# Kernel optimization log

Hardware: AMD Instinct MI355X
Metric: run time of the kernel (lower is better)

## Reference

```python
import jax, jax.numpy as jnp
import numpy as np

N_NODES = 102400
N_EDGES = 1638400
IN_SIZE = 128
OUT_SIZE = 128
G_SIZE = 100


def setup_inputs() -> dict:
    key = jax.random.key(0)
    ks = jax.random.split(key, 8)
    x = jax.random.normal(ks[0], (N_NODES, IN_SIZE), dtype=jnp.float32)
    W1 = jax.random.normal(ks[1], (IN_SIZE, OUT_SIZE), dtype=jnp.float32) * (IN_SIZE ** -0.5)
    b1 = jnp.zeros((OUT_SIZE,), dtype=jnp.float32)
    W2 = jax.random.normal(ks[2], (OUT_SIZE, OUT_SIZE), dtype=jnp.float32) * (OUT_SIZE ** -0.5)
    b2 = jnp.zeros((OUT_SIZE,), dtype=jnp.float32)
    W3 = jax.random.normal(ks[3], (OUT_SIZE, OUT_SIZE), dtype=jnp.float32) * (OUT_SIZE ** -0.5)
    b3 = jnp.zeros((OUT_SIZE,), dtype=jnp.float32)
    edge_src = jax.random.randint(ks[4], (N_EDGES,), 0, N_NODES, dtype=jnp.int64)
    edge_dst = jax.random.randint(ks[5], (N_EDGES,), 0, N_NODES, dtype=jnp.int64)
    return {"x": x, "W1": W1, "b1": b1, "W2": W2, "b2": b2, "W3": W3, "b3": b3,
            "edge_src": edge_src, "edge_dst": edge_dst, "g_size": G_SIZE}


def _degree_norm(idx, n_nodes):
    # DGL norm='both': deg.clamp(min=1) ** -0.5
    deg = jax.ops.segment_sum(jnp.ones(idx.shape, dtype=jnp.float32), idx, num_segments=n_nodes)
    return jnp.maximum(deg, 1.0) ** -0.5  # [N]


def _graph_conv(feat, W, b, edge_src, edge_dst, src_norm, dst_norm):
    # out = D_dst^{-1/2} A (D_src^{-1/2} feat) W + b
    h = feat * src_norm[:, None]                                   # [N, d]
    agg = jax.ops.segment_sum(h[edge_src], edge_dst, num_segments=feat.shape[0])  # SpMM gather+scatter
    agg = agg * dst_norm[:, None]
    return agg @ W + b


def reference(x, W1, b1, W2, b2, W3, b3, edge_src, edge_dst, g_size):
    n = x.shape[0]
    src_norm = _degree_norm(edge_src, n)  # out-degree based
    dst_norm = _degree_norm(edge_dst, n)  # in-degree based

    y1 = jax.nn.elu(_graph_conv(x, W1, b1, edge_src, edge_dst, src_norm, dst_norm))
    y2 = jax.nn.elu(_graph_conv(y1, W2, b2, edge_src, edge_dst, src_norm, dst_norm))
    y3 = jax.nn.softmax(_graph_conv(y2, W3, b3, edge_src, edge_dst, src_norm, dst_norm), axis=1)

    d = y1.shape[-1]
    return (y1.reshape(-1, g_size, d), y2.reshape(-1, g_size, d), y3.reshape(-1, g_size, d))
```

## Files before the change

kernel.cpp:

```cpp
#include <hip/hip_runtime.h>
#include <hip/hip_fp16.h>
#include <cstdint>
#include <cstddef>

#define N_NODES 102400
#define N_EDGES 1638400
#define DIM 128
#define SLOTS 48
#define NB 200
#define BKT_CAP 9216
#define SC_BLOCKS 400
#define SC_EPT 16

typedef _Float16 f16x8 __attribute__((ext_vector_type(8)));
typedef float f32x4 __attribute__((ext_vector_type(4)));


__global__ void k_initcur(int* __restrict__ dstCur, int* __restrict__ srcCur,
                          unsigned short* __restrict__ fbA,
                          unsigned short* __restrict__ fbB) {
  const int i = threadIdx.x;
  if (i < NB) {
    dstCur[i] = i * BKT_CAP;
    srcCur[i] = i * BKT_CAP;
  }
  if (i < 64) {
    reinterpret_cast<unsigned*>(fbA + (size_t)N_NODES * DIM)[i] = 0u;
  } else if (i < 128) {
    reinterpret_cast<unsigned*>(fbB + (size_t)N_NODES * DIM)[i - 64] = 0u;
  }
}

__global__ __launch_bounds__(256) void k_scatter(
    const int* __restrict__ esrc, const int* __restrict__ edst,
    int* __restrict__ dstCur, int* __restrict__ srcCur,
    unsigned* __restrict__ dstStage, unsigned short* __restrict__ srcStage) {
  __shared__ int histD[NB], histS[NB], baseD[NB], baseS[NB], locD[NB], locS[NB];
  const int tid = threadIdx.x;
  const int ebase = blockIdx.x * (256 * SC_EPT);

  for (int i = tid; i < NB; i += 256) {
    histD[i] = 0; histS[i] = 0; locD[i] = 0; locS[i] = 0;
  }
  __syncthreads();

  int s[SC_EPT], d[SC_EPT];
  #pragma unroll
  for (int k = 0; k < SC_EPT; ++k) {
    const int e = ebase + k * 256 + tid;
    s[k] = esrc[e];
    d[k] = edst[e];
    atomicAdd(&histD[d[k] >> 9], 1);
    atomicAdd(&histS[s[k] >> 9], 1);
  }
  __syncthreads();

  for (int i = tid; i < NB; i += 256) {
    baseD[i] = atomicAdd(&dstCur[i], histD[i]);
    baseS[i] = atomicAdd(&srcCur[i], histS[i]);
  }
  __syncthreads();

  #pragma unroll
  for (int k = 0; k < SC_EPT; ++k) {
    const int bd = d[k] >> 9;
    const int od = atomicAdd(&locD[bd], 1);
    dstStage[baseD[bd] + od] = ((unsigned)s[k] << 9) | (unsigned)(d[k] & 511);
    const int bs = s[k] >> 9;
    const int os = atomicAdd(&locS[bs], 1);
    srcStage[baseS[bs] + os] = (unsigned short)(s[k] & 511);
  }
}

__global__ __launch_bounds__(256) void k_csr(
    const unsigned* __restrict__ dstStage, const int* __restrict__ dstCur,
    int* __restrict__ cnt, unsigned* __restrict__ csr) {
  __shared__ int c[512], cur[512];
  const int b = blockIdx.x;
  const int tid = threadIdx.x;
  const int node0 = b * 512;

  const unsigned dummy = (unsigned)N_NODES << 8;
  uint4 dv;
  dv.x = dummy; dv.y = dummy; dv.z = dummy; dv.w = dummy;
  uint4* c4 = reinterpret_cast<uint4*>(csr + (size_t)node0 * SLOTS);
  for (int i = tid; i < 512 * SLOTS / 4; i += 256) c4[i] = dv;

  #pragma unroll
  for (int k = 0; k < 2; ++k) { c[tid + k * 256] = 0; cur[tid + k * 256] = 0; }
  __syncthreads();

  const int base = b * BKT_CAP;
  const int n = dstCur[b] - base;
  for (int i = tid; i < n; i += 256) {
    atomicAdd(&c[dstStage[base + i] & 511], 1);
  }
  __syncthreads();

  #pragma unroll
  for (int k = 0; k < 2; ++k) cnt[node0 + tid + k * 256] = c[tid + k * 256];

  for (int i = tid; i < n; i += 256) {
    const unsigned e = dstStage[base + i];
    const int dloc = (int)(e & 511u);
    const int slot = atomicAdd(&cur[dloc], 1);
    csr[(size_t)(node0 + dloc) * SLOTS + slot] = (e >> 9) << 8;
  }
}

__global__ __launch_bounds__(256) void k_sdeg(
    const unsigned short* __restrict__ srcStage, const int* __restrict__ srcCur,
    int* __restrict__ deg_src) {
  __shared__ int c[512];
  const int b = blockIdx.x;
  const int tid = threadIdx.x;
  #pragma unroll
  for (int k = 0; k < 2; ++k) c[tid + k * 256] = 0;
  __syncthreads();
  const int base = b * BKT_CAP;
  const int n = srcCur[b] - base;
  for (int i = tid; i < n; i += 256) {
    atomicAdd(&c[srcStage[base + i]], 1);
  }
  __syncthreads();
  const int node0 = b * 512;
  #pragma unroll
  for (int k = 0; k < 2; ++k) deg_src[node0 + tid + k * 256] = c[tid + k * 256];
}

__global__ void k_cvt_scale(const float* __restrict__ x,
                            const int* __restrict__ deg_src,
                            unsigned short* __restrict__ out) {
  const int i = blockIdx.x * blockDim.x + threadIdx.x;
  const int row = i >> 5;
  const int dg = deg_src[row];
  const float sn = rsqrtf((float)(dg > 0 ? dg : 1));
  const float4 v = reinterpret_cast<const float4*>(x)[i];
  ushort4 o;
  o.x = __half_as_ushort(__float2half_rn(v.x * sn));
  o.y = __half_as_ushort(__float2half_rn(v.y * sn));
  o.z = __half_as_ushort(__float2half_rn(v.z * sn));
  o.w = __half_as_ushort(__float2half_rn(v.w * sn));
  reinterpret_cast<ushort4*>(out)[i] = o;
}

template <int ACT>
__global__ __launch_bounds__(256, 6) void k_layer_m(
    const unsigned short* __restrict__ fb_in, const float* __restrict__ W,
    const float* __restrict__ bias, const int* __restrict__ cnt,
    const unsigned* __restrict__ csr, const int* __restrict__ deg_src,
    float* __restrict__ out, unsigned short* __restrict__ fb_out) {
  __shared__ float buf[32][132];
  __half* aggH = reinterpret_cast<__half*>(&buf[0][0]);

  const int tid  = threadIdx.x;
  const int lane = tid & 63;
  const int wid  = tid >> 6;
  const int q    = lane >> 4;
  const int li   = lane & 15;
  const int brow = blockIdx.x * 32;
  const char* fbase = reinterpret_cast<const char*>(fb_in);

  int c_[8];
  unsigned pk_[8];
  #pragma unroll
  for (int k = 0; k < 8; ++k) {
    const int gr = brow + wid + 4 * k;
    c_[k] = cnt[gr];
    pk_[k] = (lane < SLOTS) ? csr[(size_t)gr * SLOTS + lane] : 0u;
  }

  #pragma unroll
  for (int pass = 0; pass < 2; ++pass) {
    const int kb = pass * 4;
    __half2 acc[4][4];
    #pragma unroll
    for (int k = 0; k < 4; ++k)
      #pragma unroll
      for (int i = 0; i < 4; ++i) acc[k][i] = __float2half2_rn(0.0f);

    int cmax = c_[kb] > c_[kb + 1] ? c_[kb] : c_[kb + 1];
    cmax = cmax > c_[kb + 2] ? cmax : c_[kb + 2];
    cmax = cmax > c_[kb + 3] ? cmax : c_[kb + 3];
    cmax = cmax > SLOTS ? SLOTS : cmax;
    const int nq = (cmax + 3) >> 2;

    #pragma unroll 2
    for (int j = 0; j < nq; ++j) {
      const int sl = 4 * j + q;
      #pragma unroll
      for (int k = 0; k < 4; ++k) {
        const int o = __shfl((int)pk_[kb + k], sl);
        const uint4 v = *reinterpret_cast<const uint4*>(
            fbase + (size_t)(unsigned)o + (li << 4));
        acc[k][0] = __hadd2(acc[k][0], *reinterpret_cast<const __half2*>(&v.x));
        acc[k][1] = __hadd2(acc[k][1], *reinterpret_cast<const __half2*>(&v.y));
        acc[k][2] = __hadd2(acc[k][2], *reinterpret_cast<const __half2*>(&v.z));
        acc[k][3] = __hadd2(acc[k][3], *reinterpret_cast<const __half2*>(&v.w));
      }
    }

    #pragma unroll
    for (int k = 0; k < 4; ++k) {
      #pragma unroll
      for (int i = 0; i < 4; ++i) {
        int t = __shfl_xor(*reinterpret_cast<int*>(&acc[k][i]), 32);
        acc[k][i] = __hadd2(acc[k][i], *reinterpret_cast<__half2*>(&t));
        t = __shfl_xor(*reinterpret_cast<int*>(&acc[k][i]), 16);
        acc[k][i] = __hadd2(acc[k][i], *reinterpret_cast<__half2*>(&t));
      }
      if (q == 0) {
        const int cc = c_[kb + k];
        const __half2 dn = __float2half2_rn(rsqrtf((float)(cc > 0 ? cc : 1)));
        uint4 s;
        __half2 h;
        h = __hmul2(acc[k][0], dn); s.x = *reinterpret_cast<unsigned*>(&h);
        h = __hmul2(acc[k][1], dn); s.y = *reinterpret_cast<unsigned*>(&h);
        h = __hmul2(acc[k][2], dn); s.z = *reinterpret_cast<unsigned*>(&h);
        h = __hmul2(acc[k][3], dn); s.w = *reinterpret_cast<unsigned*>(&h);
        *reinterpret_cast<uint4*>(
            aggH + (size_t)(wid + 4 * (kb + k)) * 136 + li * 8) = s;
      }
    }
  }
  __syncthreads();

  f32x4 acc00 = {0.f, 0.f, 0.f, 0.f};
  f32x4 acc01 = {0.f, 0.f, 0.f, 0.f};
  f32x4 acc10 = {0.f, 0.f, 0.f, 0.f};
  f32x4 acc11 = {0.f, 0.f, 0.f, 0.f};
  const int colbase = wid * 32 + li;

  #pragma unroll
  for (int kc = 0; kc < 4; ++kc) {
    const int k0 = kc * 32 + q * 8;
    const f16x8 a0 = *reinterpret_cast<const f16x8*>(aggH + (size_t)li * 136 + k0);
    const f16x8 a1 =
        *reinterpret_cast<const f16x8*>(aggH + (size_t)(16 + li) * 136 + k0);
    const float* w0 = W + (size_t)k0 * DIM + colbase;
    f16x8 b0, b1;
    #pragma unroll
    for (int e = 0; e < 8; ++e) {
      b0[e] = (_Float16)w0[e * DIM];
      b1[e] = (_Float16)w0[e * DIM + 16];
    }
    acc00 = __builtin_amdgcn_mfma_f32_16x16x32_f16(a0, b0, acc00, 0, 0, 0);
    acc01 = __builtin_amdgcn_mfma_f32_16x16x32_f16(a0, b1, acc01, 0, 0, 0);
    acc10 = __builtin_amdgcn_mfma_f32_16x16x32_f16(a1, b0, acc10, 0, 0, 0);
    acc11 = __builtin_amdgcn_mfma_f32_16x16x32_f16(a1, b1, acc11, 0, 0, 0);
  }
  __syncthreads();

  #pragma unroll
  for (int r = 0; r < 4; ++r) {
    const int row0 = q * 4 + r;
    buf[row0][colbase] = acc00[r];
    buf[row0][colbase + 16] = acc01[r];
    buf[row0 + 16][colbase] = acc10[r];
    buf[row0 + 16][colbase + 16] = acc11[r];
  }
  __syncthreads();

  const int tc = tid & 31;
  const int tr = tid >> 5;
  const int c0 = tc << 2;
  const float4 bv = *reinterpret_cast<const float4*>(bias + c0);
  #pragma unroll
  for (int i = 0; i < 4; ++i) {
    const int row = tr * 4 + i;
    float4 v = *reinterpret_cast<const float4*>(&buf[row][c0]);
    v.x += bv.x; v.y += bv.y; v.z += bv.z; v.w += bv.w;
    if (ACT == 0) {
      v.x = v.x > 0.f ? v.x : expm1f(v.x);
      v.y = v.y > 0.f ? v.y : expm1f(v.y);
      v.z = v.z > 0.f ? v.z : expm1f(v.z);
      v.w = v.w > 0.f ? v.w : expm1f(v.w);
    } else {
      float m = fmaxf(fmaxf(v.x, v.y), fmaxf(v.z, v.w));
      #pragma unroll
      for (int off = 16; off >= 1; off >>= 1) m = fmaxf(m, __shfl_xor(m, off));
      v.x = expf(v.x - m);
      v.y = expf(v.y - m);
      v.z = expf(v.z - m);
      v.w = expf(v.w - m);
      float s = v.x + v.y + v.z + v.w;
      #pragma unroll
      for (int off = 16; off >= 1; off >>= 1) s += __shfl_xor(s, off);
      const float inv = 1.0f / s;
      v.x *= inv; v.y *= inv; v.z *= inv; v.w *= inv;
    }
    const size_t grow = (size_t)(brow + row);
    *reinterpret_cast<float4*>(out + grow * DIM + c0) = v;
    if (ACT == 0 && fb_out != nullptr) {
      const int dg = deg_src[grow];
      const float sn = rsqrtf((float)(dg > 0 ? dg : 1));
      ushort4 o;
      o.x = __half_as_ushort(__float2half_rn(v.x * sn));
      o.y = __half_as_ushort(__float2half_rn(v.y * sn));
      o.z = __half_as_ushort(__float2half_rn(v.z * sn));
      o.w = __half_as_ushort(__float2half_rn(v.w * sn));
      *reinterpret_cast<ushort4*>(fb_out + grow * DIM + c0) = o;
    }
  }
}

__global__ void k_dummyfill(unsigned* __restrict__ csr,
                            unsigned short* __restrict__ fbA,
                            unsigned short* __restrict__ fbB) {
  const unsigned dummy = (unsigned)N_NODES << 8;
  uint4 dv;
  dv.x = dummy; dv.y = dummy; dv.z = dummy; dv.w = dummy;
  const int i = blockIdx.x * blockDim.x + threadIdx.x;
  if (i < N_NODES * SLOTS / 4) reinterpret_cast<uint4*>(csr)[i] = dv;
  if (i < 64) reinterpret_cast<unsigned*>(fbA + (size_t)N_NODES * DIM)[i] = 0u;
  else if (i < 128)
    reinterpret_cast<unsigned*>(fbB + (size_t)N_NODES * DIM)[i - 64] = 0u;
}

__global__ void k_build(const int* __restrict__ esrc, const int* __restrict__ edst,
                        int* __restrict__ deg_src, int* __restrict__ cnt,
                        unsigned* __restrict__ csr) {
  const int i = blockIdx.x * blockDim.x + threadIdx.x;
  if (i < N_EDGES) {
    const int s = esrc[i];
    const int d = edst[i];
    atomicAdd(&deg_src[s], 1);
    const int pos = atomicAdd(&cnt[d], 1);
    csr[(size_t)d * SLOTS + pos] = (unsigned)s << 8;
  }
}

static inline size_t align1k(size_t x) { return (x + 1023) & ~(size_t)1023; }

extern "C" void kernel_launch(void* const* d_in, const int* in_sizes, int n_in,
                              void* d_out, int out_size, void* d_ws,
                              size_t ws_size, hipStream_t stream) {
  const float* x  = (const float*)d_in[0];
  const float* W1 = (const float*)d_in[1];
  const float* b1 = (const float*)d_in[2];
  const float* W2 = (const float*)d_in[3];
  const float* b2 = (const float*)d_in[4];
  const float* W3 = (const float*)d_in[5];
  const float* b3 = (const float*)d_in[6];
  const int* esrc = (const int*)d_in[7];
  const int* edst = (const int*)d_in[8];

  float* y1 = (float*)d_out;
  float* y2 = y1 + (size_t)N_NODES * DIM;
  float* y3 = y2 + (size_t)N_NODES * DIM;

  const size_t fb_bytes = (size_t)(N_NODES + 1) * DIM * 2;

  {
    char* ws = (char*)d_ws;
    int* dstCur = (int*)ws;                 ws += align1k(NB * 4);
    int* srcCur = (int*)ws;                 ws += align1k(NB * 4);
    int* cnt = (int*)ws;                    ws += align1k((size_t)N_NODES * 4);
    int* deg_src = (int*)ws;                ws += align1k((size_t)N_NODES * 4);
    unsigned* csr = (unsigned*)ws;          ws += align1k((size_t)N_NODES * SLOTS * 4);
    unsigned* dstStage = (unsigned*)ws;     ws += align1k((size_t)NB * BKT_CAP * 4);
    unsigned short* srcStage = (unsigned short*)ws;
                                            ws += align1k((size_t)NB * BKT_CAP * 2);
    unsigned short* fbA = (unsigned short*)ws;  ws += align1k(fb_bytes);
    unsigned short* fbB = (unsigned short*)ws;  ws += align1k(fb_bytes);
    const size_t need_v2 = (size_t)(ws - (char*)d_ws);

    if (ws_size >= need_v2) {
      k_initcur<<<1, 256, 0, stream>>>(dstCur, srcCur, fbA, fbB);
      k_scatter<<<SC_BLOCKS, 256, 0, stream>>>(esrc, edst, dstCur, srcCur,
                                               dstStage, srcStage);
      k_csr<<<NB, 256, 0, stream>>>(dstStage, dstCur, cnt, csr);
      k_sdeg<<<NB, 256, 0, stream>>>(srcStage, srcCur, deg_src);
      k_cvt_scale<<<N_NODES * DIM / 4 / 256, 256, 0, stream>>>(x, deg_src, fbA);

      k_layer_m<0><<<N_NODES / 32, 256, 0, stream>>>(
          fbA, W1, b1, cnt, csr, deg_src, y1, fbB);
      k_layer_m<0><<<N_NODES / 32, 256, 0, stream>>>(
          fbB, W2, b2, cnt, csr, deg_src, y2, fbA);
      k_layer_m<1><<<N_NODES / 32, 256, 0, stream>>>(
          fbA, W3, b3, cnt, csr, deg_src, y3, nullptr);
      return;
    }
  }

  {
    char* ws = (char*)d_ws;
    int* cnt     = (int*)ws;  ws += (size_t)N_NODES * 4;
    int* deg_src = (int*)ws;  ws += (size_t)N_NODES * 4;
    unsigned* csr = (unsigned*)ws;  ws += (size_t)N_NODES * SLOTS * 4;
    unsigned short* fbA = (unsigned short*)ws;  ws += align1k(fb_bytes);
    unsigned short* fbB = (unsigned short*)ws;  ws += align1k(fb_bytes);

    (void)hipMemsetAsync(cnt, 0, (size_t)N_NODES * 2 * sizeof(int), stream);
    k_dummyfill<<<(N_NODES * SLOTS / 4 + 255) / 256, 256, 0, stream>>>(csr, fbA,
                                                                       fbB);
    k_build<<<(N_EDGES + 255) / 256, 256, 0, stream>>>(esrc, edst, deg_src,
                                                       cnt, csr);
    k_cvt_scale<<<N_NODES * DIM / 4 / 256, 256, 0, stream>>>(x, deg_src, fbA);

    k_layer_m<0><<<N_NODES / 32, 256, 0, stream>>>(
        fbA, W1, b1, cnt, csr, deg_src, y1, fbB);
    k_layer_m<0><<<N_NODES / 32, 256, 0, stream>>>(
        fbB, W2, b2, cnt, csr, deg_src, y2, fbA);
    k_layer_m<1><<<N_NODES / 32, 256, 0, stream>>>(
        fbA, W3, b3, cnt, csr, deg_src, y3, nullptr);
  }
}
```

Before: 296.0 us.

## Sort destination nodes by in-degree so layer blocks have balanced neighbor counts

Adds a counting sort of destination nodes by in-degree (histogram, scan, order kernels) and makes each layer block process 32 nodes of similar degree through an indirection array. Each pass loops to the maximum neighbor count of its 4 rows, so grouping similar degrees is meant to cut padded iterations wasted on dummy slots. In exchange, output row writes and csr/cnt reads become scattered rather than contiguous, and three small kernels are added to the pipeline.

```diff
diff --git a/kernel.cpp b/kernel.cpp
--- a/kernel.cpp
+++ b/kernel.cpp
@@ -11,6 +11,7 @@
 #define BKT_CAP 9216
 #define SC_BLOCKS 400
 #define SC_EPT 16
+#define DBINS 64
 
 typedef _Float16 f16x8 __attribute__((ext_vector_type(8)));
 typedef float f32x4 __attribute__((ext_vector_type(4)));
@@ -18,7 +19,8 @@
 
 __global__ void k_initcur(int* __restrict__ dstCur, int* __restrict__ srcCur,
                           unsigned short* __restrict__ fbA,
-                          unsigned short* __restrict__ fbB) {
+                          unsigned short* __restrict__ fbB,
+                          int* __restrict__ binCnt) {
   const int i = threadIdx.x;
   if (i < NB) {
     dstCur[i] = i * BKT_CAP;
@@ -28,6 +30,8 @@
     reinterpret_cast<unsigned*>(fbA + (size_t)N_NODES * DIM)[i] = 0u;
   } else if (i < 128) {
     reinterpret_cast<unsigned*>(fbB + (size_t)N_NODES * DIM)[i - 64] = 0u;
+  } else if (i < 128 + DBINS) {
+    binCnt[i - 128] = 0;
   }
 }
 
@@ -126,6 +130,51 @@
   const int node0 = b * 512;
   #pragma unroll
   for (int k = 0; k < 2; ++k) deg_src[node0 + tid + k * 256] = c[tid + k * 256];
+}
+
+__global__ __launch_bounds__(256) void k_dhist(const int* __restrict__ cnt,
+                                               int* __restrict__ binCnt) {
+  __shared__ int h[DBINS];
+  const int tid = threadIdx.x;
+  if (tid < DBINS) h[tid] = 0;
+  __syncthreads();
+  const int node = blockIdx.x * 256 + tid;
+  int d = cnt[node];
+  d = d > (DBINS - 1) ? (DBINS - 1) : d;
+  atomicAdd(&h[d], 1);
+  __syncthreads();
+  if (tid < DBINS) atomicAdd(&binCnt[tid], h[tid]);
+}
+
+__global__ void k_dscan(const int* __restrict__ binCnt,
+                        int* __restrict__ binCur) {
+  const int lane = threadIdx.x;
+  const int v = binCnt[lane];
+  int s = v;
+  #pragma unroll
+  for (int off = 1; off < 64; off <<= 1) {
+    const int t = __shfl_up(s, off);
+    if (lane >= off) s += t;
+  }
+  binCur[lane] = s - v;
+}
+
+__global__ __launch_bounds__(256) void k_dorder(const int* __restrict__ cnt,
+                                                int* __restrict__ binCur,
+                                                unsigned* __restrict__ order) {
+  __shared__ int h[DBINS], base[DBINS], loc[DBINS];
+  const int tid = threadIdx.x;
+  if (tid < DBINS) { h[tid] = 0; loc[tid] = 0; }
+  __syncthreads();
+  const int node = blockIdx.x * 256 + tid;
+  int d = cnt[node];
+  d = d > (DBINS - 1) ? (DBINS - 1) : d;
+  atomicAdd(&h[d], 1);
+  __syncthreads();
+  if (tid < DBINS) base[tid] = atomicAdd(&binCur[tid], h[tid]);
+  __syncthreads();
+  const int o = atomicAdd(&loc[d], 1);
+  order[base[d] + o] = (unsigned)node;
 }
 
 __global__ void k_cvt_scale(const float* __restrict__ x,
@@ -149,8 +198,10 @@
     const unsigned short* __restrict__ fb_in, const float* __restrict__ W,
     const float* __restrict__ bias, const int* __restrict__ cnt,
     const unsigned* __restrict__ csr, const int* __restrict__ deg_src,
-    float* __restrict__ out, unsigned short* __restrict__ fb_out) {
+    const unsigned* __restrict__ order, float* __restrict__ out,
+    unsigned short* __restrict__ fb_out) {
   __shared__ float buf[32][132];
+  __shared__ unsigned nodes[32];
   __half* aggH = reinterpret_cast<__half*>(&buf[0][0]);
 
   const int tid  = threadIdx.x;
@@ -161,11 +212,14 @@
   const int brow = blockIdx.x * 32;
   const char* fbase = reinterpret_cast<const char*>(fb_in);
 
+  if (tid < 32) nodes[tid] = order[brow + tid];
+  __syncthreads();
+
   int c_[8];
   unsigned pk_[8];
   #pragma unroll
   for (int k = 0; k < 8; ++k) {
-    const int gr = brow + wid + 4 * k;
+    const int gr = (int)nodes[wid + 4 * k];
     c_[k] = cnt[gr];
     pk_[k] = (lane < SLOTS) ? csr[(size_t)gr * SLOTS + lane] : 0u;
   }
@@ -289,7 +343,7 @@
       const float inv = 1.0f / s;
       v.x *= inv; v.y *= inv; v.z *= inv; v.w *= inv;
     }
-    const size_t grow = (size_t)(brow + row);
+    const size_t grow = (size_t)nodes[row];
     *reinterpret_cast<float4*>(out + grow * DIM + c0) = v;
     if (ACT == 0 && fb_out != nullptr) {
       const int dg = deg_src[grow];
@@ -306,7 +360,8 @@
 
 __global__ void k_dummyfill(unsigned* __restrict__ csr,
                             unsigned short* __restrict__ fbA,
-                            unsigned short* __restrict__ fbB) {
+                            unsigned short* __restrict__ fbB,
+                            int* __restrict__ binCnt) {
   const unsigned dummy = (unsigned)N_NODES << 8;
   uint4 dv;
   dv.x = dummy; dv.y = dummy; dv.z = dummy; dv.w = dummy;
@@ -315,6 +370,8 @@
   if (i < 64) reinterpret_cast<unsigned*>(fbA + (size_t)N_NODES * DIM)[i] = 0u;
   else if (i < 128)
     reinterpret_cast<unsigned*>(fbB + (size_t)N_NODES * DIM)[i - 64] = 0u;
+  else if (i < 128 + DBINS)
+    binCnt[i - 128] = 0;
 }
 
 __global__ void k_build(const int* __restrict__ esrc, const int* __restrict__ edst,
@@ -355,8 +412,11 @@
     char* ws = (char*)d_ws;
     int* dstCur = (int*)ws;                 ws += align1k(NB * 4);
     int* srcCur = (int*)ws;                 ws += align1k(NB * 4);
+    int* binCnt = (int*)ws;                 ws += align1k(DBINS * 4);
+    int* binCur = (int*)ws;                 ws += align1k(DBINS * 4);
     int* cnt = (int*)ws;                    ws += align1k((size_t)N_NODES * 4);
     int* deg_src = (int*)ws;                ws += align1k((size_t)N_NODES * 4);
+    unsigned* order = (unsigned*)ws;        ws += align1k((size_t)N_NODES * 4);
     unsigned* csr = (unsigned*)ws;          ws += align1k((size_t)N_NODES * SLOTS * 4);
     unsigned* dstStage = (unsigned*)ws;     ws += align1k((size_t)NB * BKT_CAP * 4);
     unsigned short* srcStage = (unsigned short*)ws;
@@ -366,19 +426,22 @@
     const size_t need_v2 = (size_t)(ws - (char*)d_ws);
 
     if (ws_size >= need_v2) {
-      k_initcur<<<1, 256, 0, stream>>>(dstCur, srcCur, fbA, fbB);
+      k_initcur<<<1, 256, 0, stream>>>(dstCur, srcCur, fbA, fbB, binCnt);
       k_scatter<<<SC_BLOCKS, 256, 0, stream>>>(esrc, edst, dstCur, srcCur,
                                                dstStage, srcStage);
       k_csr<<<NB, 256, 0, stream>>>(dstStage, dstCur, cnt, csr);
       k_sdeg<<<NB, 256, 0, stream>>>(srcStage, srcCur, deg_src);
+      k_dhist<<<N_NODES / 256, 256, 0, stream>>>(cnt, binCnt);
+      k_dscan<<<1, 64, 0, stream>>>(binCnt, binCur);
+      k_dorder<<<N_NODES / 256, 256, 0, stream>>>(cnt, binCur, order);
       k_cvt_scale<<<N_NODES * DIM / 4 / 256, 256, 0, stream>>>(x, deg_src, fbA);
 
       k_layer_m<0><<<N_NODES / 32, 256, 0, stream>>>(
-          fbA, W1, b1, cnt, csr, deg_src, y1, fbB);
+          fbA, W1, b1, cnt, csr, deg_src, order, y1, fbB);
       k_layer_m<0><<<N_NODES / 32, 256, 0, stream>>>(
-          fbB, W2, b2, cnt, csr, deg_src, y2, fbA);
+          fbB, W2, b2, cnt, csr, deg_src, order, y2, fbA);
       k_layer_m<1><<<N_NODES / 32, 256, 0, stream>>>(
-          fbA, W3, b3, cnt, csr, deg_src, y3, nullptr);
+          fbA, W3, b3, cnt, csr, deg_src, order, y3, nullptr);
       return;
     }
   }
@@ -387,22 +450,28 @@
     char* ws = (char*)d_ws;
     int* cnt     = (int*)ws;  ws += (size_t)N_NODES * 4;
     int* deg_src = (int*)ws;  ws += (size_t)N_NODES * 4;
+    int* binCnt = (int*)ws;   ws += align1k(DBINS * 4);
+    int* binCur = (int*)ws;   ws += align1k(DBINS * 4);
+    unsigned* order = (unsigned*)ws;  ws += align1k((size_t)N_NODES * 4);
     unsigned* csr = (unsigned*)ws;  ws += (size_t)N_NODES * SLOTS * 4;
     unsigned short* fbA = (unsigned short*)ws;  ws += align1k(fb_bytes);
     unsigned short* fbB = (unsigned short*)ws;  ws += align1k(fb_bytes);
 
     (void)hipMemsetAsync(cnt, 0, (size_t)N_NODES * 2 * sizeof(int), stream);
-    k_dummyfill<<<(N_NODES * SLOTS / 4 + 255) / 256, 256, 0, stream>>>(csr, fbA,
-                                                                       fbB);
+    k_dummyfill<<<(N_NODES * SLOTS / 4 + 255) / 256, 256, 0, stream>>>(
+        csr, fbA, fbB, binCnt);
     k_build<<<(N_EDGES + 255) / 256, 256, 0, stream>>>(esrc, edst, deg_src,
                                                        cnt, csr);
+    k_dhist<<<N_NODES / 256, 256, 0, stream>>>(cnt, binCnt);
+    k_dscan<<<1, 64, 0, stream>>>(binCnt, binCur);
+    k_dorder<<<N_NODES / 256, 256, 0, stream>>>(cnt, binCur, order);
     k_cvt_scale<<<N_NODES * DIM / 4 / 256, 256, 0, stream>>>(x, deg_src, fbA);
 
     k_layer_m<0><<<N_NODES / 32, 256, 0, stream>>>(
-        fbA, W1, b1, cnt, csr, deg_src, y1, fbB);
+        fbA, W1, b1, cnt, csr, deg_src, order, y1, fbB);
     k_layer_m<0><<<N_NODES / 32, 256, 0, stream>>>(
-        fbB, W2, b2, cnt, csr, deg_src, y2, fbA);
+        fbB, W2, b2, cnt, csr, deg_src, order, y2, fbA);
     k_layer_m<1><<<N_NODES / 32, 256, 0, stream>>>(
-        fbA, W3, b3, cnt, csr, deg_src, y3, nullptr);
-  }
-}
+        fbA, W3, b3, cnt, csr, deg_src, order, y3, nullptr);
+  }
+}
```

After: 322.0 us. 1.09x slower.

## Pre-transpose weights to fp16, merge source-degree count into CSR kernel, raise occupancy

Applied to the files above, without the earlier changes.

A new kernel converts W1/W2/W3 once per call into transposed fp16 layout, so each layer kernel loads B fragments as contiguous 16-byte vectors. This replaces the sixteen strided fp32 loads and conversions per MFMA step. The separate source-degree histogram kernel is folded into the CSR build kernel, which removes one launch. Launch bounds for the layer kernel rise from 6 to 8 blocks per SM, which may limit registers and cause spills.

```diff
diff --git a/kernel.cpp b/kernel.cpp
--- a/kernel.cpp
+++ b/kernel.cpp
@@ -31,6 +31,19 @@
   }
 }
 
+__global__ void k_cvt_w(const float* __restrict__ W1,
+                        const float* __restrict__ W2,
+                        const float* __restrict__ W3,
+                        _Float16* __restrict__ Wt) {
+  const int i = blockIdx.x * 256 + threadIdx.x;
+  const int w = i >> 14;
+  const int r = i & 16383;
+  const int col = r >> 7;
+  const int k = r & 127;
+  const float* W = (w == 0) ? W1 : ((w == 1) ? W2 : W3);
+  Wt[i] = (_Float16)W[k * DIM + col];
+}
+
 __global__ __launch_bounds__(256) void k_scatter(
     const int* __restrict__ esrc, const int* __restrict__ edst,
     int* __restrict__ dstCur, int* __restrict__ srcCur,
@@ -74,8 +87,10 @@
 
 __global__ __launch_bounds__(256) void k_csr(
     const unsigned* __restrict__ dstStage, const int* __restrict__ dstCur,
-    int* __restrict__ cnt, unsigned* __restrict__ csr) {
-  __shared__ int c[512], cur[512];
+    const unsigned short* __restrict__ srcStage, const int* __restrict__ srcCur,
+    int* __restrict__ cnt, unsigned* __restrict__ csr,
+    int* __restrict__ deg_src) {
+  __shared__ int c[512], cur[512], cs[512];
   const int b = blockIdx.x;
   const int tid = threadIdx.x;
   const int node0 = b * 512;
@@ -87,7 +102,11 @@
   for (int i = tid; i < 512 * SLOTS / 4; i += 256) c4[i] = dv;
 
   #pragma unroll
-  for (int k = 0; k < 2; ++k) { c[tid + k * 256] = 0; cur[tid + k * 256] = 0; }
+  for (int k = 0; k < 2; ++k) {
+    c[tid + k * 256] = 0;
+    cur[tid + k * 256] = 0;
+    cs[tid + k * 256] = 0;
+  }
   __syncthreads();
 
   const int base = b * BKT_CAP;
@@ -95,10 +114,17 @@
   for (int i = tid; i < n; i += 256) {
     atomicAdd(&c[dstStage[base + i] & 511], 1);
   }
-  __syncthreads();
-
-  #pragma unroll
-  for (int k = 0; k < 2; ++k) cnt[node0 + tid + k * 256] = c[tid + k * 256];
+  const int ns = srcCur[b] - base;
+  for (int i = tid; i < ns; i += 256) {
+    atomicAdd(&cs[srcStage[base + i]], 1);
+  }
+  __syncthreads();
+
+  #pragma unroll
+  for (int k = 0; k < 2; ++k) {
+    cnt[node0 + tid + k * 256] = c[tid + k * 256];
+    deg_src[node0 + tid + k * 256] = cs[tid + k * 256];
+  }
 
   for (int i = tid; i < n; i += 256) {
     const unsigned e = dstStage[base + i];
@@ -106,26 +132,6 @@
     const int slot = atomicAdd(&cur[dloc], 1);
     csr[(size_t)(node0 + dloc) * SLOTS + slot] = (e >> 9) << 8;
   }
-}
-
-__global__ __launch_bounds__(256) void k_sdeg(
-    const unsigned short* __restrict__ srcStage, const int* __restrict__ srcCur,
-    int* __restrict__ deg_src) {
-  __shared__ int c[512];
-  const int b = blockIdx.x;
-  const int tid = threadIdx.x;
-  #pragma unroll
-  for (int k = 0; k < 2; ++k) c[tid + k * 256] = 0;
-  __syncthreads();
-  const int base = b * BKT_CAP;
-  const int n = srcCur[b] - base;
-  for (int i = tid; i < n; i += 256) {
-    atomicAdd(&c[srcStage[base + i]], 1);
-  }
-  __syncthreads();
-  const int node0 = b * 512;
-  #pragma unroll
-  for (int k = 0; k < 2; ++k) deg_src[node0 + tid + k * 256] = c[tid + k * 256];
 }
 
 __global__ void k_cvt_scale(const float* __restrict__ x,
@@ -145,8 +151,8 @@
 }
 
 template <int ACT>
-__global__ __launch_bounds__(256, 6) void k_layer_m(
-    const unsigned short* __restrict__ fb_in, const float* __restrict__ W,
+__global__ __launch_bounds__(256, 8) void k_layer_m(
+    const unsigned short* __restrict__ fb_in, const _Float16* __restrict__ Wt,
     const float* __restrict__ bias, const int* __restrict__ cnt,
     const unsigned* __restrict__ csr, const int* __restrict__ deg_src,
     float* __restrict__ out, unsigned short* __restrict__ fb_out) {
@@ -230,6 +236,7 @@
   f32x4 acc10 = {0.f, 0.f, 0.f, 0.f};
   f32x4 acc11 = {0.f, 0.f, 0.f, 0.f};
   const int colbase = wid * 32 + li;
+  const _Float16* wt0 = Wt + (size_t)colbase * DIM;
 
   #pragma unroll
   for (int kc = 0; kc < 4; ++kc) {
@@ -237,13 +244,8 @@
     const f16x8 a0 = *reinterpret_cast<const f16x8*>(aggH + (size_t)li * 136 + k0);
     const f16x8 a1 =
         *reinterpret_cast<const f16x8*>(aggH + (size_t)(16 + li) * 136 + k0);
-    const float* w0 = W + (size_t)k0 * DIM + colbase;
-    f16x8 b0, b1;
-    #pragma unroll
-    for (int e = 0; e < 8; ++e) {
-      b0[e] = (_Float16)w0[e * DIM];
-      b1[e] = (_Float16)w0[e * DIM + 16];
-    }
+    const f16x8 b0 = *reinterpret_cast<const f16x8*>(wt0 + k0);
+    const f16x8 b1 = *reinterpret_cast<const f16x8*>(wt0 + 16 * DIM + k0);
     acc00 = __builtin_amdgcn_mfma_f32_16x16x32_f16(a0, b0, acc00, 0, 0, 0);
     acc01 = __builtin_amdgcn_mfma_f32_16x16x32_f16(a0, b1, acc01, 0, 0, 0);
     acc10 = __builtin_amdgcn_mfma_f32_16x16x32_f16(a1, b0, acc10, 0, 0, 0);
@@ -355,6 +357,7 @@
     char* ws = (char*)d_ws;
     int* dstCur = (int*)ws;                 ws += align1k(NB * 4);
     int* srcCur = (int*)ws;                 ws += align1k(NB * 4);
+    _Float16* Wt3 = (_Float16*)ws;          ws += align1k(3 * 16384 * 2);
     int* cnt = (int*)ws;                    ws += align1k((size_t)N_NODES * 4);
     int* deg_src = (int*)ws;                ws += align1k((size_t)N_NODES * 4);
     unsigned* csr = (unsigned*)ws;          ws += align1k((size_t)N_NODES * SLOTS * 4);
@@ -367,18 +370,19 @@
 
     if (ws_size >= need_v2) {
       k_initcur<<<1, 256, 0, stream>>>(dstCur, srcCur, fbA, fbB);
+      k_cvt_w<<<192, 256, 0, stream>>>(W1, W2, W3, Wt3);
       k_scatter<<<SC_BLOCKS, 256, 0, stream>>>(esrc, edst, dstCur, srcCur,
                                                dstStage, srcStage);
-      k_csr<<<NB, 256, 0, stream>>>(dstStage, dstCur, cnt, csr);
-      k_sdeg<<<NB, 256, 0, stream>>>(srcStage, srcCur, deg_src);
+      k_csr<<<NB, 256, 0, stream>>>(dstStage, dstCur, srcStage, srcCur, cnt,
+                                    csr, deg_src);
       k_cvt_scale<<<N_NODES * DIM / 4 / 256, 256, 0, stream>>>(x, deg_src, fbA);
 
       k_layer_m<0><<<N_NODES / 32, 256, 0, stream>>>(
-          fbA, W1, b1, cnt, csr, deg_src, y1, fbB);
+          fbA, Wt3, b1, cnt, csr, deg_src, y1, fbB);
       k_layer_m<0><<<N_NODES / 32, 256, 0, stream>>>(
-          fbB, W2, b2, cnt, csr, deg_src, y2, fbA);
+          fbB, Wt3 + 16384, b2, cnt, csr, deg_src, y2, fbA);
       k_layer_m<1><<<N_NODES / 32, 256, 0, stream>>>(
-          fbA, W3, b3, cnt, csr, deg_src, y3, nullptr);
+          fbA, Wt3 + 32768, b3, cnt, csr, deg_src, y3, nullptr);
       return;
     }
   }
@@ -387,6 +391,7 @@
     char* ws = (char*)d_ws;
     int* cnt     = (int*)ws;  ws += (size_t)N_NODES * 4;
     int* deg_src = (int*)ws;  ws += (size_t)N_NODES * 4;
+    _Float16* Wt3 = (_Float16*)ws;  ws += align1k(3 * 16384 * 2);
     unsigned* csr = (unsigned*)ws;  ws += (size_t)N_NODES * SLOTS * 4;
     unsigned short* fbA = (unsigned short*)ws;  ws += align1k(fb_bytes);
     unsigned short* fbB = (unsigned short*)ws;  ws += align1k(fb_bytes);
@@ -394,15 +399,16 @@
     (void)hipMemsetAsync(cnt, 0, (size_t)N_NODES * 2 * sizeof(int), stream);
     k_dummyfill<<<(N_NODES * SLOTS / 4 + 255) / 256, 256, 0, stream>>>(csr, fbA,
                                                                        fbB);
+    k_cvt_w<<<192, 256, 0, stream>>>(W1, W2, W3, Wt3);
     k_build<<<(N_EDGES + 255) / 256, 256, 0, stream>>>(esrc, edst, deg_src,
                                                        cnt, csr);
     k_cvt_scale<<<N_NODES * DIM / 4 / 256, 256, 0, stream>>>(x, deg_src, fbA);
 
     k_layer_m<0><<<N_NODES / 32, 256, 0, stream>>>(
-        fbA, W1, b1, cnt, csr, deg_src, y1, fbB);
+        fbA, Wt3, b1, cnt, csr, deg_src, y1, fbB);
     k_layer_m<0><<<N_NODES / 32, 256, 0, stream>>>(
-        fbB, W2, b2, cnt, csr, deg_src, y2, fbA);
+        fbB, Wt3 + 16384, b2, cnt, csr, deg_src, y2, fbA);
     k_layer_m<1><<<N_NODES / 32, 256, 0, stream>>>(
-        fbA, W3, b3, cnt, csr, deg_src, y3, nullptr);
-  }
-}
+        fbA, Wt3 + 32768, b3, cnt, csr, deg_src, y3, nullptr);
+  }
+}
```

Result: no change. 300.4 us (+1.5%).
